# Performance work log

Measured on AMD Instinct MI355X. Metric: run time of the kernel, lower is better.

The kernel has to match this reference:

```python
import jax, jax.numpy as jnp
import numpy as np

N_NODES = 100000
N_EDGES = 1600000
NFEAT, NHID, NCLASS = 64, 128, 32


def _glorot(key, shape):
    fan_in, fan_out = shape[0], shape[1]
    lim = np.sqrt(6.0 / (fan_in + fan_out))
    return jax.random.uniform(key, shape, jnp.float32, -lim, lim)


def setup_inputs() -> dict:
    key = jax.random.key(0)
    ks = jax.random.split(key, 12)
    x = jax.random.normal(ks[0], (N_NODES, NFEAT), jnp.float32)
    edge_idx = jax.random.randint(ks[1], (2, N_EDGES), 0, N_NODES, jnp.int64)
    edge_weight = jax.random.uniform(ks[2], (N_EDGES,), jnp.float32)
    return {
        "x": x,
        "edge_idx": edge_idx,
        "edge_weight": edge_weight,
        # SAGEConv 1: out = mean_agg(x) @ Wl1 + b1 + x @ Wr1
        "Wl1": _glorot(ks[3], (NFEAT, NHID)),
        "Wr1": _glorot(ks[4], (NFEAT, NHID)),
        "b1": jnp.zeros((NHID,), jnp.float32),
        # SAGEConv 2
        "Wl2": _glorot(ks[5], (NHID, NHID)),
        "Wr2": _glorot(ks[6], (NHID, NHID)),
        "b2": jnp.zeros((NHID,), jnp.float32),
        # fc head: Linear(nhid, nclass) -> Linear(nclass, 1)
        "Wfc1": _glorot(ks[7], (NHID, NCLASS)),
        "bfc1": jnp.zeros((NCLASS,), jnp.float32),
        "Wfc2": _glorot(ks[8], (NCLASS, 1)),
        "bfc2": jnp.zeros((1,), jnp.float32),
    }


def _sage_conv(x, src, dst, Wl, Wr, b, n_nodes):
    # mean aggregation of source features at destination nodes
    msg_sum = jax.ops.segment_sum(x[src], dst, num_segments=n_nodes)  # [N, d]
    deg = jax.ops.segment_sum(jnp.ones((src.shape[0], 1), x.dtype), dst,
                              num_segments=n_nodes)                    # [N, 1]
    mean = msg_sum / jnp.maximum(deg, 1.0)
    return mean @ Wl + b + x @ Wr


def reference(x, edge_idx, edge_weight, Wl1, Wr1, b1, Wl2, Wr2, b2,
              Wfc1, bfc1, Wfc2, bfc2):
    n_nodes = x.shape[0]
    src, dst = edge_idx[0], edge_idx[1]
    # dropout is identity in eval mode (training=False)
    h = _sage_conv(x, src, dst, Wl1, Wr1, b1, n_nodes)   # [N, nhid]
    h = _sage_conv(h, src, dst, Wl2, Wr2, b2, n_nodes)   # [N, nhid]
    h = h @ Wfc1 + bfc1                                   # [N, nclass]
    out = h @ Wfc2 + bfc2                                 # [N, 1]
    return out
```

## Files before the change

### kernel.cpp

```cpp
#include <hip/hip_runtime.h>

#define S_SHIFT 8
#define S_NODES 256
#define NBKT    400
#define CAP     5120
#define CHUNK   4096
#define EPT     8
#define NREP    4

__global__ __launch_bounds__(512) void prep_kernel(
    const float* __restrict__ x,
    const int* __restrict__ src, const int* __restrict__ dst,
    int E, int N, int B,
    int* __restrict__ cursor, unsigned* __restrict__ bucket,
    const float* __restrict__ Wl1, const float* __restrict__ Wr1, const float* __restrict__ b1,
    const float* __restrict__ Wl2, const float* __restrict__ Wr2, const float* __restrict__ b2,
    const float* __restrict__ Wfc1, const float* __restrict__ bfc1,
    const float* __restrict__ Wfc2, const float* __restrict__ bfc2,
    float* __restrict__ ga, float2* __restrict__ gbc, float* __restrict__ c01)
{
    __shared__ int hist[NBKT], lbase[NBKT], lcur[NBKT];
    __shared__ float wv[192], uu[128], vl2[128], vr2[128], w2[32];
    int t = threadIdx.x;
    int l = t & 63;
    int w = t >> 6;

    if (t < 32) w2[t] = Wfc2[t];
    __syncthreads();
    for (int j = 0; j < 16; ++j) {
        int i = w + 8 * j;
        float p = (l < 32) ? Wfc1[i * 32 + l] * w2[l] : 0.f;
        for (int m = 16; m; m >>= 1) p += __shfl_xor(p, m);
        if (l == 0) uu[i] = p;
    }
    __syncthreads();
    for (int j = 0; j < 16; ++j) {
        int i = w + 8 * j;
        float ua = uu[l], ub = uu[64 + l];
        float pa = Wl2[i * 128 + l] * ua + Wl2[i * 128 + 64 + l] * ub;
        float pb = Wr2[i * 128 + l] * ua + Wr2[i * 128 + 64 + l] * ub;
        for (int m = 32; m; m >>= 1) { pa += __shfl_xor(pa, m); pb += __shfl_xor(pb, m); }
        if (l == 0) { vl2[i] = pa; vr2[i] = pb; }
    }
    __syncthreads();
    for (int j = 0; j < 8; ++j) {
        int i = w + 8 * j;
        float l1a = Wl1[i * 128 + l], l1b = Wl1[i * 128 + 64 + l];
        float r1a = Wr1[i * 128 + l], r1b = Wr1[i * 128 + 64 + l];
        float La = vl2[l], Lb = vl2[64 + l], Ra = vr2[l], Rb = vr2[64 + l];
        float pc = l1a * La + l1b * Lb;
        float pb = l1a * Ra + l1b * Rb + r1a * La + r1b * Lb;
        float pa = r1a * Ra + r1b * Rb;
        for (int m = 32; m; m >>= 1) {
            pa += __shfl_xor(pa, m); pb += __shfl_xor(pb, m); pc += __shfl_xor(pc, m);
        }
        if (l == 0) { wv[i] = pa; wv[64 + i] = pb; wv[128 + i] = pc; }
    }
    if (blockIdx.x == 0 && w == 7) {
        float p0 = b1[l] * vr2[l] + b1[64 + l] * vr2[64 + l]
                 + b2[l] * uu[l] + b2[64 + l] * uu[64 + l];
        if (l < 32) p0 += bfc1[l] * w2[l];
        float p1 = b1[l] * vl2[l] + b1[64 + l] * vl2[64 + l];
        for (int m = 32; m; m >>= 1) { p0 += __shfl_xor(p0, m); p1 += __shfl_xor(p1, m); }
        if (l == 0) { c01[0] = p0 + bfc2[0]; c01[1] = p1; }
    }

    {
        int e0 = blockIdx.x * CHUNK;
        int cnt = E - e0; if (cnt > CHUNK) cnt = CHUNK;
        int sd[EPT], ss[EPT];
        for (int i = t; i < B; i += 512) hist[i] = 0;
        __syncthreads();
        for (int k = 0; k < EPT; ++k) {
            int i = t + k * 512;
            if (i < cnt) {
                sd[k] = dst[e0 + i];
                ss[k] = src[e0 + i];
                atomicAdd(&hist[sd[k] >> S_SHIFT], 1);
            }
        }
        __syncthreads();
        for (int i = t; i < B; i += 512) {
            lcur[i] = 0;
            if (hist[i] > 0) lbase[i] = atomicAdd(&cursor[i], hist[i]);
        }
        __syncthreads();
        for (int k = 0; k < EPT; ++k) {
            int i = t + k * 512;
            if (i < cnt) {
                int bb = sd[k] >> S_SHIFT;
                int off = atomicAdd(&lcur[bb], 1);
                bucket[(size_t)bb * CAP + (unsigned)(lbase[bb] + off)] =
                    ((unsigned)ss[k] << S_SHIFT) | (unsigned)(sd[k] & (S_NODES - 1));
            }
        }
    }

    {
        int fp = l & 15, sub = l >> 4;
        float4 wa4 = ((const float4*)wv)[fp];
        float4 wb4 = ((const float4*)wv)[16 + fp];
        float4 wc4 = ((const float4*)wv)[32 + fp];
        const float4* x4 = (const float4*)x;
        int Q = (N + 3) >> 2;
        int stride = gridDim.x * 8;
        for (int qd = blockIdx.x * 8 + w; qd < Q; qd += stride) {
            int node = qd * 4 + sub;
            float a = 0.f, b = 0.f, c = 0.f;
            if (node < N) {
                float4 v = x4[(size_t)node * 16 + fp];
                a = v.x * wa4.x + v.y * wa4.y + v.z * wa4.z + v.w * wa4.w;
                b = v.x * wb4.x + v.y * wb4.y + v.z * wb4.z + v.w * wb4.w;
                c = v.x * wc4.x + v.y * wc4.y + v.z * wc4.z + v.w * wc4.w;
            }
            for (int m = 8; m; m >>= 1) {
                a += __shfl_xor(a, m); b += __shfl_xor(b, m); c += __shfl_xor(c, m);
            }
            if (fp == 0 && node < N) { ga[node] = a; gbc[node] = make_float2(b, c); }
        }
    }
}

__global__ __launch_bounds__(512) void aggA_kernel(
    const unsigned* __restrict__ bucket, const int* __restrict__ cursor,
    const float2* __restrict__ gbc, const float* __restrict__ ga,
    const float* __restrict__ c01,
    float* __restrict__ q, float* __restrict__ t1, float* __restrict__ inv, int N)
{
    __shared__ float aB[NREP][S_NODES], aC[NREP][S_NODES];
    __shared__ int cnt[NREP][S_NODES];
    int t = threadIdx.x, b = blockIdx.x;
    int r = (t >> 6) & (NREP - 1);
    float* aBf = (float*)aB; float* aCf = (float*)aC; int* cnf = (int*)cnt;
    for (int i = t; i < NREP * S_NODES; i += 512) { aBf[i] = 0.f; aCf[i] = 0.f; cnf[i] = 0; }
    __syncthreads();
    int n = cursor[b];
    const unsigned* bp = bucket + (size_t)b * CAP;
    for (int i = t; i < n; i += 512) {
        unsigned uu = bp[i];
        float2 g = gbc[uu >> S_SHIFT];
        int dl = uu & (S_NODES - 1);
        atomicAdd(&aB[r][dl], g.x);
        atomicAdd(&aC[r][dl], g.y);
        atomicAdd(&cnt[r][dl], 1);
    }
    __syncthreads();
    if (t < S_NODES) {
        int node = (b << S_SHIFT) + t;
        if (node < N) {
            float sb = aB[0][t] + aB[1][t] + aB[2][t] + aB[3][t];
            float sc = aC[0][t] + aC[1][t] + aC[2][t] + aC[3][t];
            int d = cnt[0][t] + cnt[1][t] + cnt[2][t] + cnt[3][t];
            float iv = 1.0f / ((d > 0) ? (float)d : 1.0f);
            inv[node] = iv;
            q[node]   = iv * sc;
            t1[node]  = ga[node] + iv * sb + c01[0] + (d > 0 ? c01[1] : 0.f);
        }
    }
}

__global__ __launch_bounds__(512) void aggB_kernel(
    const unsigned* __restrict__ bucket, const int* __restrict__ cursor,
    const float* __restrict__ q, const float* __restrict__ t1,
    const float* __restrict__ inv, float* __restrict__ out, int N)
{
    __shared__ float a2[NREP][S_NODES];
    int t = threadIdx.x, b = blockIdx.x;
    int r = (t >> 6) & (NREP - 1);
    float* a2f = (float*)a2;
    for (int i = t; i < NREP * S_NODES; i += 512) a2f[i] = 0.f;
    __syncthreads();
    int n = cursor[b];
    const unsigned* bp = bucket + (size_t)b * CAP;
    for (int i = t; i < n; i += 512) {
        unsigned uu = bp[i];
        atomicAdd(&a2[r][uu & (S_NODES - 1)], q[uu >> S_SHIFT]);
    }
    __syncthreads();
    if (t < S_NODES) {
        int node = (b << S_SHIFT) + t;
        if (node < N)
            out[node] = t1[node] + inv[node] * (a2[0][t] + a2[1][t] + a2[2][t] + a2[3][t]);
    }
}

extern "C" void kernel_launch(void* const* d_in, const int* in_sizes, int n_in,
                              void* d_out, int out_size, void* d_ws, size_t ws_size,
                              hipStream_t stream) {
    const float* x    = (const float*)d_in[0];
    const int*   eidx = (const int*)d_in[1];
    const float* Wl1  = (const float*)d_in[3];
    const float* Wr1  = (const float*)d_in[4];
    const float* b1   = (const float*)d_in[5];
    const float* Wl2  = (const float*)d_in[6];
    const float* Wr2  = (const float*)d_in[7];
    const float* b2   = (const float*)d_in[8];
    const float* Wfc1 = (const float*)d_in[9];
    const float* bfc1 = (const float*)d_in[10];
    const float* Wfc2 = (const float*)d_in[11];
    const float* bfc2 = (const float*)d_in[12];

    const int N = in_sizes[0] / 64;
    const int E = in_sizes[2];
    const int* src = eidx;
    const int* dst = eidx + E;
    const int B = (N + S_NODES - 1) / S_NODES;
    const int nprep = (E + CHUNK - 1) / CHUNK;

    char* ws = (char*)d_ws;
    int*      cursor = (int*)(ws);
    float*    c01    = (float*)(ws + 2048);
    float*    ga     = (float*)(ws + 4096);
    float*    q      = (float*)(ws + 4096 + (size_t)N * 4);
    float*    t1     = (float*)(ws + 4096 + (size_t)N * 8);
    float*    inv    = (float*)(ws + 4096 + (size_t)N * 12);
    float2*   gbc    = (float2*)(ws + 4096 + (size_t)N * 16);
    unsigned* bucket = (unsigned*)(ws + 4096 + (size_t)N * 24);

    hipMemsetAsync(cursor, 0, 2048, stream);

    prep_kernel<<<nprep, 512, 0, stream>>>(
        x, src, dst, E, N, B, cursor, bucket,
        Wl1, Wr1, b1, Wl2, Wr2, b2, Wfc1, bfc1, Wfc2, bfc2,
        ga, gbc, c01);

    aggA_kernel<<<B, 512, 0, stream>>>(bucket, cursor, gbc, ga, c01, q, t1, inv, N);
    aggB_kernel<<<B, 512, 0, stream>>>(bucket, cursor, q, t1, inv, (float*)d_out, N);
}
```

Baseline: 174.6 us.

## Stage bucketed edges in LDS for coalesced scatter and widen buckets to 512 nodes

The prep kernel now sorts each chunk's edges by bucket in shared memory, using a block-wide prefix scan over the bucket histogram. It then writes each bucket's run out contiguously, replacing per-edge scattered global stores. Buckets double to 512 destination nodes, which halves the bucket count and the global cursor atomics. The aggregation kernels move to 1024-thread blocks to match. The price is extra scan synchronisation in prep and only about 196 aggregation blocks, which may leave some CUs idle.

After: 176.4 us. No clear change (+1.1%).

```diff
diff --git a/kernel.cpp b/kernel.cpp
--- a/kernel.cpp
+++ b/kernel.cpp
@@ -1,9 +1,8 @@
 #include <hip/hip_runtime.h>
 
-#define S_SHIFT 8
-#define S_NODES 256
-#define NBKT    400
-#define CAP     5120
+#define S_SHIFT 9
+#define S_NODES 512
+#define CAP     10240
 #define CHUNK   4096
 #define EPT     8
 #define NREP    4
@@ -19,7 +18,9 @@
     const float* __restrict__ Wfc2, const float* __restrict__ bfc2,
     float* __restrict__ ga, float2* __restrict__ gbc, float* __restrict__ c01)
 {
-    __shared__ int hist[NBKT], lbase[NBKT], lcur[NBKT];
+    __shared__ unsigned stage[CHUNK];
+    __shared__ unsigned char bn8[CHUNK];
+    __shared__ int hist[256], scan[256], obase[256], lcur[256], lbase[256];
     __shared__ float wv[192], uu[128], vl2[128], vr2[128], w2[32];
     int t = threadIdx.x;
     int l = t & 63;
@@ -69,7 +70,7 @@
         int e0 = blockIdx.x * CHUNK;
         int cnt = E - e0; if (cnt > CHUNK) cnt = CHUNK;
         int sd[EPT], ss[EPT];
-        for (int i = t; i < B; i += 512) hist[i] = 0;
+        if (t < 256) hist[t] = 0;
         __syncthreads();
         for (int k = 0; k < EPT; ++k) {
             int i = t + k * 512;
@@ -80,19 +81,35 @@
             }
         }
         __syncthreads();
-        for (int i = t; i < B; i += 512) {
-            lcur[i] = 0;
-            if (hist[i] > 0) lbase[i] = atomicAdd(&cursor[i], hist[i]);
+        if (t < 256) scan[t] = hist[t];
+        __syncthreads();
+        for (int off = 1; off < 256; off <<= 1) {
+            int tmp = 0;
+            if (t < 256 && t >= off) tmp = scan[t - off];
+            __syncthreads();
+            if (t < 256) scan[t] += tmp;
+            __syncthreads();
+        }
+        if (t < 256) {
+            int ob = scan[t] - hist[t];
+            obase[t] = ob;
+            lcur[t] = ob;
+            if (t < B && hist[t] > 0) lbase[t] = atomicAdd(&cursor[t], hist[t]);
         }
         __syncthreads();
         for (int k = 0; k < EPT; ++k) {
             int i = t + k * 512;
             if (i < cnt) {
                 int bb = sd[k] >> S_SHIFT;
-                int off = atomicAdd(&lcur[bb], 1);
-                bucket[(size_t)bb * CAP + (unsigned)(lbase[bb] + off)] =
-                    ((unsigned)ss[k] << S_SHIFT) | (unsigned)(sd[k] & (S_NODES - 1));
-            }
+                int pos = atomicAdd(&lcur[bb], 1);
+                stage[pos] = ((unsigned)ss[k] << S_SHIFT) | (unsigned)(sd[k] & (S_NODES - 1));
+                bn8[pos] = (unsigned char)bb;
+            }
+        }
+        __syncthreads();
+        for (int i = t; i < cnt; i += 512) {
+            int bb = bn8[i];
+            bucket[(size_t)bb * CAP + (unsigned)(lbase[bb] + (i - obase[bb]))] = stage[i];
         }
     }
 
@@ -121,7 +138,7 @@
     }
 }
 
-__global__ __launch_bounds__(512) void aggA_kernel(
+__global__ __launch_bounds__(1024) void aggA_kernel(
     const unsigned* __restrict__ bucket, const int* __restrict__ cursor,
     const float2* __restrict__ gbc, const float* __restrict__ ga,
     const float* __restrict__ c01,
@@ -132,11 +149,11 @@
     int t = threadIdx.x, b = blockIdx.x;
     int r = (t >> 6) & (NREP - 1);
     float* aBf = (float*)aB; float* aCf = (float*)aC; int* cnf = (int*)cnt;
-    for (int i = t; i < NREP * S_NODES; i += 512) { aBf[i] = 0.f; aCf[i] = 0.f; cnf[i] = 0; }
+    for (int i = t; i < NREP * S_NODES; i += 1024) { aBf[i] = 0.f; aCf[i] = 0.f; cnf[i] = 0; }
     __syncthreads();
     int n = cursor[b];
     const unsigned* bp = bucket + (size_t)b * CAP;
-    for (int i = t; i < n; i += 512) {
+    for (int i = t; i < n; i += 1024) {
         unsigned uu = bp[i];
         float2 g = gbc[uu >> S_SHIFT];
         int dl = uu & (S_NODES - 1);
@@ -159,7 +176,7 @@
     }
 }
 
-__global__ __launch_bounds__(512) void aggB_kernel(
+__global__ __launch_bounds__(1024) void aggB_kernel(
     const unsigned* __restrict__ bucket, const int* __restrict__ cursor,
     const float* __restrict__ q, const float* __restrict__ t1,
     const float* __restrict__ inv, float* __restrict__ out, int N)
@@ -168,11 +185,11 @@
     int t = threadIdx.x, b = blockIdx.x;
     int r = (t >> 6) & (NREP - 1);
     float* a2f = (float*)a2;
-    for (int i = t; i < NREP * S_NODES; i += 512) a2f[i] = 0.f;
+    for (int i = t; i < NREP * S_NODES; i += 1024) a2f[i] = 0.f;
     __syncthreads();
     int n = cursor[b];
     const unsigned* bp = bucket + (size_t)b * CAP;
-    for (int i = t; i < n; i += 512) {
+    for (int i = t; i < n; i += 1024) {
         unsigned uu = bp[i];
         atomicAdd(&a2[r][uu & (S_NODES - 1)], q[uu >> S_SHIFT]);
     }
@@ -209,21 +226,21 @@
 
     char* ws = (char*)d_ws;
     int*      cursor = (int*)(ws);
-    float*    c01    = (float*)(ws + 2048);
-    float*    ga     = (float*)(ws + 4096);
-    float*    q      = (float*)(ws + 4096 + (size_t)N * 4);
-    float*    t1     = (float*)(ws + 4096 + (size_t)N * 8);
-    float*    inv    = (float*)(ws + 4096 + (size_t)N * 12);
-    float2*   gbc    = (float2*)(ws + 4096 + (size_t)N * 16);
-    unsigned* bucket = (unsigned*)(ws + 4096 + (size_t)N * 24);
-
-    hipMemsetAsync(cursor, 0, 2048, stream);
+    float*    c01    = (float*)(ws + 1024);
+    float*    ga     = (float*)(ws + 2048);
+    float*    q      = (float*)(ws + 2048 + (size_t)N * 4);
+    float*    t1     = (float*)(ws + 2048 + (size_t)N * 8);
+    float*    inv    = (float*)(ws + 2048 + (size_t)N * 12);
+    float2*   gbc    = (float2*)(ws + 2048 + (size_t)N * 16);
+    unsigned* bucket = (unsigned*)(ws + 2048 + (size_t)N * 24);
+
+    hipMemsetAsync(cursor, 0, 1024, stream);
 
     prep_kernel<<<nprep, 512, 0, stream>>>(
         x, src, dst, E, N, B, cursor, bucket,
         Wl1, Wr1, b1, Wl2, Wr2, b2, Wfc1, bfc1, Wfc2, bfc2,
         ga, gbc, c01);
 
-    aggA_kernel<<<B, 512, 0, stream>>>(bucket, cursor, gbc, ga, c01, q, t1, inv, N);
-    aggB_kernel<<<B, 512, 0, stream>>>(bucket, cursor, q, t1, inv, (float*)d_out, N);
-}
+    aggA_kernel<<<B, 1024, 0, stream>>>(bucket, cursor, gbc, ga, c01, q, t1, inv, N);
+    aggB_kernel<<<B, 1024, 0, stream>>>(bucket, cursor, q, t1, inv, (float*)d_out, N);
+}
```
